# Kernel optimization log

Measured on AMD Instinct MI355X. Metric: run time of the kernel, lower is better.

Reference implementation:

```python
import jax, jax.numpy as jnp
import numpy as np
from jax import lax

WINDOW_SIZE = 11
SIGMA = 1.5
C1 = 0.01 ** 2
C2 = 0.03 ** 2


def _gaussian_window(channel, window_size, sigma=SIGMA):
    x = jnp.arange(window_size, dtype=jnp.float32)
    g = jnp.exp(-((x - window_size // 2) ** 2) / (2.0 * sigma * sigma))
    g = g / g.sum()
    w2d = jnp.outer(g, g)  # [ws, ws]
    # depthwise kernel in OIHW with feature_group_count=channel: [C, 1, ws, ws]
    return jnp.broadcast_to(w2d[None, None], (channel, 1, window_size, window_size))


def _dwconv(x, window, pad, channel):
    return lax.conv_general_dilated(
        x, window, window_strides=(1, 1), padding=[(pad, pad), (pad, pad)],
        dimension_numbers=("NCHW", "OIHW", "NCHW"), feature_group_count=channel)


def setup_inputs() -> dict:
    key = jax.random.key(0)
    k1, k2 = jax.random.split(key)
    shape = (16, 3, 512, 512)
    img1 = jax.random.uniform(k1, shape, dtype=jnp.float32)
    img2 = jax.random.uniform(k2, shape, dtype=jnp.float32)
    return {"img1": img1, "img2": img2}


def reference(img1, img2):
    _, channel, height, width = img1.shape
    ws = min(WINDOW_SIZE, height, width)
    window = _gaussian_window(channel, ws).astype(img1.dtype)
    pad = WINDOW_SIZE // 2  # matches torch code: padding=window_size // 2

    mu1 = _dwconv(img1, window, pad, channel)
    mu2 = _dwconv(img2, window, pad, channel)
    mu1_sq = mu1 * mu1
    mu2_sq = mu2 * mu2
    mu1_mu2 = mu1 * mu2

    sigma1_sq = _dwconv(img1 * img1, window, pad, channel) - mu1_sq
    sigma2_sq = _dwconv(img2 * img2, window, pad, channel) - mu2_sq
    sigma12 = _dwconv(img1 * img2, window, pad, channel) - mu1_mu2

    ssim_map = ((2.0 * mu1_mu2 + C1) * (2.0 * sigma12 + C2)) / (
        (mu1_sq + mu2_sq + C1) * (sigma1_sq + sigma2_sq + C2))
    return 1.0 - ssim_map.mean()
```

## Files before the change

kernel.cpp:

```cpp
#include <hip/hip_runtime.h>
#include <hip/hip_fp16.h>


#define IMGH 512
#define IMGW 512
#define TW 64
#define TH 32
#define HRR 42
#define C1F 1.0e-4f
#define C2F 9.0e-4f
#define GX 8
#define GY 16
#define GZ 48
#define NBLOCKS (GX * GY * GZ)
#define NPIX (16 * 3 * 512 * 512)

#define W0 0.0010283818f
#define W1 0.0075987503f
#define W2 0.0360007547f
#define W3 0.1093606960f
#define W4 0.2130055367f
#define W5 0.2660117184f

struct alignas(8) H4 { __half2 ab; __half2 qc; };

static __device__ __forceinline__ __half2 pkrtz(float a, float b) {
    auto r = __builtin_amdgcn_cvt_pkrtz(a, b);
    return *reinterpret_cast<__half2*>(&r);
}

__global__ __launch_bounds__(512, 4)
void ssim_tile(const float* __restrict__ img1, const float* __restrict__ img2,
               float* __restrict__ partials) {
    __shared__ H4 sPm[HRR][64];
    __shared__ float wsum[8];

    const float W[11] = {W0, W1, W2, W3, W4, W5, W4, W3, W2, W1, W0};
    __half2 wsH[11];
#pragma unroll
    for (int i = 0; i < 11; ++i) wsH[i] = __half2half2(__float2half(W[i]));

    const int tid = threadIdx.x;
    const int r0 = blockIdx.y * TH;
    const int c0 = blockIdx.x * TW;
    const size_t pbase = (size_t)blockIdx.z * (IMGH * IMGW);
    const float* a0 = img1 + pbase;
    const float* b0 = img2 + pbase;
    const bool fast = (blockIdx.x >= 1) & (blockIdx.x <= GX - 2) &
                      (blockIdx.y >= 1) & (blockIdx.y <= GY - 2);

    if (tid < HRR * 8) {
        const int row = tid >> 3;
        const int cg  = tid & 7;
        const int gr  = r0 - 5 + row;
        const bool rowok = (unsigned)gr < IMGH;
        const int grc = rowok ? gr : 0;
        const int gc0 = c0 + 8 * cg - 8;
        const float* ra = a0 + (size_t)grc * IMGW;
        const float* rb = b0 + (size_t)grc * IMGW;

        float4 va[6], vb[6];
        if (fast) {
#pragma unroll
            for (int g = 0; g < 6; ++g)
                va[g] = *reinterpret_cast<const float4*>(ra + (gc0 + 4 * g));
#pragma unroll
            for (int g = 0; g < 6; ++g)
                vb[g] = *reinterpret_cast<const float4*>(rb + (gc0 + 4 * g));
        } else {
#pragma unroll
            for (int g = 0; g < 6; ++g) {
                int gc = gc0 + 4 * g;
                va[g] = make_float4(0.f, 0.f, 0.f, 0.f); vb[g] = va[g];
                if (rowok && (unsigned)gc < IMGW) {
                    va[g] = *reinterpret_cast<const float4*>(ra + gc);
                    vb[g] = *reinterpret_cast<const float4*>(rb + gc);
                }
            }
        }

        __half2 AB[18], QC[18];
        auto emit = [&](int t, float a, float b) {
            AB[t] = pkrtz(a, b);
            QC[t] = pkrtz(__builtin_fmaf(a, a, b * b), a * b);
        };
        emit(0, va[0].w, vb[0].w);
#pragma unroll
        for (int g = 1; g < 6; ++g) {
            int t = 4 * g - 3;
            emit(t,     va[g].x, vb[g].x);
            emit(t + 1, va[g].y, vb[g].y);
            emit(t + 2, va[g].z, vb[g].z);
            if (g < 5) emit(t + 3, va[g].w, vb[g].w);
        }

        __half2 accAB[8], accQC[8];
        const __half2 z2 = __half2half2(__float2half(0.f));
#pragma unroll
        for (int m = 0; m < 8; ++m) { accAB[m] = z2; accQC[m] = z2; }
#pragma unroll
        for (int t = 0; t < 18; ++t) {
#pragma unroll
            for (int m = 0; m < 8; ++m) {
                int k = t - m;
                if (k >= 0 && k <= 10) {
                    accAB[m] = __hfma2(wsH[k], AB[t], accAB[m]);
                    accQC[m] = __hfma2(wsH[k], QC[t], accQC[m]);
                }
            }
        }
#pragma unroll
        for (int m = 0; m < 8; ++m) {
            H4 h; h.ab = accAB[m]; h.qc = accQC[m];
            sPm[row][8 * cg + m] = h;
        }
    }
    __syncthreads();

    const int col = tid & 63;
    const int rbase = (tid >> 6) * 4;
    const H4* pm = &sPm[rbase][col];

    __half2 mAB[4], mQC[4];
    {
        const __half2 z2 = __half2half2(__float2half(0.f));
#pragma unroll
        for (int r = 0; r < 4; ++r) { mAB[r] = z2; mQC[r] = z2; }
    }
#pragma unroll
    for (int j = 0; j < 14; ++j) {
        H4 h = pm[j * 64];
#pragma unroll
        for (int r = 0; r < 4; ++r) {
            int i = j - r;
            if (i >= 0 && i <= 10) {
                mAB[r] = __hfma2(wsH[i], h.ab, mAB[r]);
                mQC[r] = __hfma2(wsH[i], h.qc, mQC[r]);
            }
        }
    }

    float lsum = 0.f;
#pragma unroll
    for (int r = 0; r < 4; ++r) {
        float2 m12 = __half22float2(mAB[r]);
        float2 qc  = __half22float2(mQC[r]);
        float mu1 = m12.x, mu2 = m12.y;
        float mu11 = mu1 * mu1, mu22 = mu2 * mu2, mu12 = mu1 * mu2;
        float s12 = qc.y - mu12;
        float num = (2.f * mu12 + C1F) * (2.f * s12 + C2F);
        float den = (mu11 + mu22 + C1F) * ((qc.x - mu11 - mu22) + C2F);
        lsum += num * __builtin_amdgcn_rcpf(den);
    }

#pragma unroll
    for (int off = 32; off > 0; off >>= 1) lsum += __shfl_down(lsum, off, 64);
    if ((tid & 63) == 0) wsum[tid >> 6] = lsum;
    __syncthreads();
    if (tid == 0) {
        float t = 0.f;
#pragma unroll
        for (int w = 0; w < 8; ++w) t += wsum[w];
        partials[((size_t)blockIdx.z * GY + blockIdx.y) * GX + blockIdx.x] = t;
    }
}

__global__ __launch_bounds__(1024)
void ssim_reduce(const float* __restrict__ partials, float* __restrict__ out, int n) {
    __shared__ float lds[1024];
    float s = 0.f;
    for (int i = threadIdx.x; i < n; i += 1024) s += partials[i];
    lds[threadIdx.x] = s;
    __syncthreads();
    for (int off = 512; off > 0; off >>= 1) {
        if ((int)threadIdx.x < off) lds[threadIdx.x] += lds[threadIdx.x + off];
        __syncthreads();
    }
    if (threadIdx.x == 0) out[0] = 1.f - lds[0] / (float)NPIX;
}

extern "C" void kernel_launch(void* const* d_in, const int* in_sizes, int n_in,
                              void* d_out, int out_size, void* d_ws, size_t ws_size,
                              hipStream_t stream) {
    const float* img1 = (const float*)d_in[0];
    const float* img2 = (const float*)d_in[1];
    float* out = (float*)d_out;
    float* partials = (float*)d_ws;

    dim3 grid(GX, GY, GZ);
    ssim_tile<<<grid, 512, 0, stream>>>(img1, img2, partials);
    ssim_reduce<<<1, 1024, 0, stream>>>(partials, out, NBLOCKS);
}
```

Baseline: 45.23 us.

## Stage packed half2 input tile in LDS with coalesced loads before horizontal pass

Input loading is split into a cooperative phase where all 512 threads load float4s of both images, pack them to half2 and store them into a new LDS tile. The horizontal pass then reads its 24 inputs from LDS, which removes the redundant overlapping global loads per thread group. The squared and cross products are now computed in fp16 from the packed values, which reduces precision compared with the earlier fp32 products. LDS stores of the partial results are widened to float4. The cost is extra LDS usage and one more barrier.

```diff
diff --git a/kernel.cpp b/kernel.cpp
--- a/kernel.cpp
+++ b/kernel.cpp
@@ -7,6 +7,7 @@
 #define TW 64
 #define TH 32
 #define HRR 42
+#define SAB_STRIDE 84
 #define C1F 1.0e-4f
 #define C2F 9.0e-4f
 #define GX 8
@@ -32,6 +33,7 @@
 __global__ __launch_bounds__(512, 4)
 void ssim_tile(const float* __restrict__ img1, const float* __restrict__ img2,
                float* __restrict__ partials) {
+    __shared__ __half2 sAB[HRR][SAB_STRIDE];
     __shared__ H4 sPm[HRR][64];
     __shared__ float wsum[8];
 
@@ -49,50 +51,43 @@
     const bool fast = (blockIdx.x >= 1) & (blockIdx.x <= GX - 2) &
                       (blockIdx.y >= 1) & (blockIdx.y <= GY - 2);
 
+    for (int t = tid; t < HRR * 20; t += 512) {
+        int row = (unsigned)t / 20u;
+        int cq  = t - row * 20;
+        int gr  = r0 - 5 + row;
+        int gc  = c0 - 8 + 4 * cq;
+        __half2 h0, h1, h2, h3;
+        if (fast || ((unsigned)gr < IMGH && (unsigned)gc < IMGW)) {
+            const float4 va = *reinterpret_cast<const float4*>(
+                a0 + (size_t)gr * IMGW + gc);
+            const float4 vb = *reinterpret_cast<const float4*>(
+                b0 + (size_t)gr * IMGW + gc);
+            h0 = pkrtz(va.x, vb.x);
+            h1 = pkrtz(va.y, vb.y);
+            h2 = pkrtz(va.z, vb.z);
+            h3 = pkrtz(va.w, vb.w);
+        } else {
+            h0 = h1 = h2 = h3 = __half2half2(__float2half(0.f));
+        }
+        float4 st;
+        reinterpret_cast<__half2*>(&st)[0] = h0;
+        reinterpret_cast<__half2*>(&st)[1] = h1;
+        reinterpret_cast<__half2*>(&st)[2] = h2;
+        reinterpret_cast<__half2*>(&st)[3] = h3;
+        *reinterpret_cast<float4*>(&sAB[row][4 * cq]) = st;
+    }
+    __syncthreads();
+
     if (tid < HRR * 8) {
         const int row = tid >> 3;
         const int cg  = tid & 7;
-        const int gr  = r0 - 5 + row;
-        const bool rowok = (unsigned)gr < IMGH;
-        const int grc = rowok ? gr : 0;
-        const int gc0 = c0 + 8 * cg - 8;
-        const float* ra = a0 + (size_t)grc * IMGW;
-        const float* rb = b0 + (size_t)grc * IMGW;
+        const __half2* pr = &sAB[row][8 * cg];
 
-        float4 va[6], vb[6];
-        if (fast) {
+        __half2 A[24];
 #pragma unroll
-            for (int g = 0; g < 6; ++g)
-                va[g] = *reinterpret_cast<const float4*>(ra + (gc0 + 4 * g));
-#pragma unroll
-            for (int g = 0; g < 6; ++g)
-                vb[g] = *reinterpret_cast<const float4*>(rb + (gc0 + 4 * g));
-        } else {
-#pragma unroll
-            for (int g = 0; g < 6; ++g) {
-                int gc = gc0 + 4 * g;
-                va[g] = make_float4(0.f, 0.f, 0.f, 0.f); vb[g] = va[g];
-                if (rowok && (unsigned)gc < IMGW) {
-                    va[g] = *reinterpret_cast<const float4*>(ra + gc);
-                    vb[g] = *reinterpret_cast<const float4*>(rb + gc);
-                }
-            }
-        }
-
-        __half2 AB[18], QC[18];
-        auto emit = [&](int t, float a, float b) {
-            AB[t] = pkrtz(a, b);
-            QC[t] = pkrtz(__builtin_fmaf(a, a, b * b), a * b);
-        };
-        emit(0, va[0].w, vb[0].w);
-#pragma unroll
-        for (int g = 1; g < 6; ++g) {
-            int t = 4 * g - 3;
-            emit(t,     va[g].x, vb[g].x);
-            emit(t + 1, va[g].y, vb[g].y);
-            emit(t + 2, va[g].z, vb[g].z);
-            if (g < 5) emit(t + 3, va[g].w, vb[g].w);
-        }
+        for (int q = 0; q < 6; ++q)
+            *reinterpret_cast<float4*>(&A[4 * q]) =
+                *reinterpret_cast<const float4*>(&pr[4 * q]);
 
         __half2 accAB[8], accQC[8];
         const __half2 z2 = __half2half2(__float2half(0.f));
@@ -100,19 +95,28 @@
         for (int m = 0; m < 8; ++m) { accAB[m] = z2; accQC[m] = z2; }
 #pragma unroll
         for (int t = 0; t < 18; ++t) {
+            __half2 ab = A[t + 3];
+            __half2 q2 = __hmul2(ab, ab);
+            __half2 qc = __halves2half2(
+                __hadd(__low2half(q2), __high2half(q2)),
+                __hmul(__low2half(ab), __high2half(ab)));
 #pragma unroll
             for (int m = 0; m < 8; ++m) {
                 int k = t - m;
                 if (k >= 0 && k <= 10) {
-                    accAB[m] = __hfma2(wsH[k], AB[t], accAB[m]);
-                    accQC[m] = __hfma2(wsH[k], QC[t], accQC[m]);
+                    accAB[m] = __hfma2(wsH[k], ab, accAB[m]);
+                    accQC[m] = __hfma2(wsH[k], qc, accQC[m]);
                 }
             }
         }
 #pragma unroll
-        for (int m = 0; m < 8; ++m) {
-            H4 h; h.ab = accAB[m]; h.qc = accQC[m];
-            sPm[row][8 * cg + m] = h;
+        for (int m = 0; m < 8; m += 2) {
+            float4 st;
+            reinterpret_cast<__half2*>(&st)[0] = accAB[m];
+            reinterpret_cast<__half2*>(&st)[1] = accQC[m];
+            reinterpret_cast<__half2*>(&st)[2] = accAB[m + 1];
+            reinterpret_cast<__half2*>(&st)[3] = accQC[m + 1];
+            *reinterpret_cast<float4*>(&sPm[row][8 * cg + m]) = st;
         }
     }
     __syncthreads();
```

Result: slower. 53.62 us (+18.5%).

## Stage input tiles into LDS via direct global-to-LDS loads with swizzle

Applied to the files above, without the earlier changes.

Replaces the per-thread register float4 global loads of the halo tile with cooperative global_load_lds (16-byte) transfers into a swizzled shared staging buffer, then reads rows back from LDS. Border tiles zero-fill the stage first. The intent is to issue wider, better-coalesced memory traffic that bypasses VGPRs and to spread loads across all 512 threads instead of the 336 that compute. It also packs the horizontal-pass stores into 16-byte LDS writes. The cost is an extra ~27KB of LDS per block, which may reduce occupancy, plus an extra barrier and an extra LDS round-trip.

```diff
diff --git a/kernel.cpp b/kernel.cpp
--- a/kernel.cpp
+++ b/kernel.cpp
@@ -15,6 +15,10 @@
 #define NBLOCKS (GX * GY * GZ)
 #define NPIX (16 * 3 * 512 * 512)
 
+#define PLANE_W 3360
+#define STAGE_W 6912
+#define STAGE_BYTES 26880
+
 #define W0 0.0010283818f
 #define W1 0.0075987503f
 #define W2 0.0360007547f
@@ -29,9 +33,16 @@
     return *reinterpret_cast<__half2*>(&r);
 }
 
+static __device__ __forceinline__ void gload16(const void* g, void* l) {
+    __builtin_amdgcn_global_load_lds(
+        (const __attribute__((address_space(1))) void*)g,
+        (__attribute__((address_space(3))) void*)l, 16, 0, 0);
+}
+
 __global__ __launch_bounds__(512, 4)
 void ssim_tile(const float* __restrict__ img1, const float* __restrict__ img2,
                float* __restrict__ partials) {
+    __shared__ float stage[STAGE_W];
     __shared__ H4 sPm[HRR][64];
     __shared__ float wsum[8];
 
@@ -49,34 +60,46 @@
     const bool fast = (blockIdx.x >= 1) & (blockIdx.x <= GX - 2) &
                       (blockIdx.y >= 1) & (blockIdx.y <= GY - 2);
 
+    if (!fast) {
+        const float4 z4 = make_float4(0.f, 0.f, 0.f, 0.f);
+        for (int t = tid; t < STAGE_W / 4; t += 512)
+            reinterpret_cast<float4*>(stage)[t] = z4;
+        __syncthreads();
+    }
+    {
+        const int wv = tid >> 6, ln = tid & 63;
+        for (int i = wv; i < 27; i += 8) {
+            int o = (i << 10) + (ln << 4);
+            if (o < STAGE_BYTES) {
+                int plane = (o >= PLANE_W * 4) ? 1 : 0;
+                int po = o - plane * (PLANE_W * 4);
+                int row = (unsigned)po / 320u;
+                int ro  = po - row * 320;
+                ro ^= ((row >> 1) & 1) << 4;
+                int gr = r0 - 5 + row;
+                int gc = c0 - 8 + (ro >> 2);
+                if (fast || ((unsigned)gr < IMGH && (unsigned)gc < IMGW)) {
+                    const float* g = (plane ? b0 : a0) + (size_t)gr * IMGW + gc;
+                    gload16(g, reinterpret_cast<char*>(stage) + (i << 10));
+                }
+            }
+        }
+    }
+    __syncthreads();
+
     if (tid < HRR * 8) {
         const int row = tid >> 3;
         const int cg  = tid & 7;
-        const int gr  = r0 - 5 + row;
-        const bool rowok = (unsigned)gr < IMGH;
-        const int grc = rowok ? gr : 0;
-        const int gc0 = c0 + 8 * cg - 8;
-        const float* ra = a0 + (size_t)grc * IMGW;
-        const float* rb = b0 + (size_t)grc * IMGW;
+        const int s4  = ((row >> 1) & 1) << 2;
+        const float* pa = stage + row * 80 + cg * 8;
+        const float* pb = pa + PLANE_W;
 
         float4 va[6], vb[6];
-        if (fast) {
-#pragma unroll
-            for (int g = 0; g < 6; ++g)
-                va[g] = *reinterpret_cast<const float4*>(ra + (gc0 + 4 * g));
-#pragma unroll
-            for (int g = 0; g < 6; ++g)
-                vb[g] = *reinterpret_cast<const float4*>(rb + (gc0 + 4 * g));
-        } else {
-#pragma unroll
-            for (int g = 0; g < 6; ++g) {
-                int gc = gc0 + 4 * g;
-                va[g] = make_float4(0.f, 0.f, 0.f, 0.f); vb[g] = va[g];
-                if (rowok && (unsigned)gc < IMGW) {
-                    va[g] = *reinterpret_cast<const float4*>(ra + gc);
-                    vb[g] = *reinterpret_cast<const float4*>(rb + gc);
-                }
-            }
+#pragma unroll
+        for (int q = 0; q < 6; ++q) {
+            int off = ((q << 2) ^ s4);
+            va[q] = *reinterpret_cast<const float4*>(pa + off);
+            vb[q] = *reinterpret_cast<const float4*>(pb + off);
         }
 
         __half2 AB[18], QC[18];
@@ -110,9 +133,13 @@
             }
         }
 #pragma unroll
-        for (int m = 0; m < 8; ++m) {
-            H4 h; h.ab = accAB[m]; h.qc = accQC[m];
-            sPm[row][8 * cg + m] = h;
+        for (int m = 0; m < 8; m += 2) {
+            float4 st;
+            reinterpret_cast<__half2*>(&st)[0] = accAB[m];
+            reinterpret_cast<__half2*>(&st)[1] = accQC[m];
+            reinterpret_cast<__half2*>(&st)[2] = accAB[m + 1];
+            reinterpret_cast<__half2*>(&st)[3] = accQC[m + 1];
+            *reinterpret_cast<float4*>(&sPm[row][8 * cg + m]) = st;
         }
     }
     __syncthreads();
```

New measurement: 55.97 us. +23.7%, slower.

## Compute separable Gaussian convolutions with MFMA banded-matrix products

Applied to the files above, without the earlier changes.

Replaces the packed-half FMA horizontal and vertical 11-tap passes with MFMA 16x16x32 f16 matrix multiplies, using a banded Toeplitz weight matrix built from a zero-padded shared weight array. Inputs are staged into shared memory as four f16 planes (a, b, a²+b², ab), then transposed intermediate planes feed the vertical pass. The aim is to move the convolution arithmetic from vector ALUs onto the matrix cores. In exchange it uses more LDS, adds an extra barrier and layout transposes with possible bank conflicts, and relies on intricate fragment indexing.

```diff
diff --git a/kernel.cpp b/kernel.cpp
--- a/kernel.cpp
+++ b/kernel.cpp
@@ -6,14 +6,20 @@
 #define IMGW 512
 #define TW 64
 #define TH 32
-#define HRR 42
-#define C1F 1.0e-4f
-#define C2F 9.0e-4f
 #define GX 8
 #define GY 16
 #define GZ 48
 #define NBLOCKS (GX * GY * GZ)
 #define NPIX (16 * 3 * 512 * 512)
+#define C1F 1.0e-4f
+#define C2F 9.0e-4f
+
+#define INROWS 42
+#define INSTRIDE 88
+#define INPLANE (INROWS * INSTRIDE)
+#define VSTRIDE 44
+#define VPLANE (64 * VSTRIDE)
+#define WBASE 34
 
 #define W0 0.0010283818f
 #define W1 0.0075987503f
@@ -22,7 +28,8 @@
 #define W4 0.2130055367f
 #define W5 0.2660117184f
 
-struct alignas(8) H4 { __half2 ab; __half2 qc; };
+typedef _Float16 half8v __attribute__((ext_vector_type(8)));
+typedef float f32x4 __attribute__((ext_vector_type(4)));
 
 static __device__ __forceinline__ __half2 pkrtz(float a, float b) {
     auto r = __builtin_amdgcn_cvt_pkrtz(a, b);
@@ -32,15 +39,14 @@
 __global__ __launch_bounds__(512, 4)
 void ssim_tile(const float* __restrict__ img1, const float* __restrict__ img2,
                float* __restrict__ partials) {
-    __shared__ H4 sPm[HRR][64];
+    __shared__ _Float16 sWext[96];
+    __shared__ _Float16 sIn[4 * INPLANE];
+    __shared__ _Float16 sV[4 * VPLANE];
     __shared__ float wsum[8];
 
-    const float W[11] = {W0, W1, W2, W3, W4, W5, W4, W3, W2, W1, W0};
-    __half2 wsH[11];
-#pragma unroll
-    for (int i = 0; i < 11; ++i) wsH[i] = __half2half2(__float2half(W[i]));
-
-    const int tid = threadIdx.x;
+    const int tid  = threadIdx.x;
+    const int lane = tid & 63;
+    const int wv   = tid >> 6;
     const int r0 = blockIdx.y * TH;
     const int c0 = blockIdx.x * TW;
     const size_t pbase = (size_t)blockIdx.z * (IMGH * IMGW);
@@ -49,113 +55,112 @@
     const bool fast = (blockIdx.x >= 1) & (blockIdx.x <= GX - 2) &
                       (blockIdx.y >= 1) & (blockIdx.y <= GY - 2);
 
-    if (tid < HRR * 8) {
-        const int row = tid >> 3;
-        const int cg  = tid & 7;
-        const int gr  = r0 - 5 + row;
-        const bool rowok = (unsigned)gr < IMGH;
-        const int grc = rowok ? gr : 0;
-        const int gc0 = c0 + 8 * cg - 8;
-        const float* ra = a0 + (size_t)grc * IMGW;
-        const float* rb = b0 + (size_t)grc * IMGW;
+    if (tid < 96) {
+        const float W[11] = {W0, W1, W2, W3, W4, W5, W4, W3, W2, W1, W0};
+        float w = 0.f;
+#pragma unroll
+        for (int j = 0; j < 11; ++j) w = (tid == WBASE + j) ? W[j] : w;
+        sWext[tid] = (_Float16)w;
+    }
 
-        float4 va[6], vb[6];
-        if (fast) {
+    auto prep = [&](int qid) {
+        const int row = qid / 20;
+        const int cq  = qid - row * 20;
+        const int gr = r0 - 5 + row;
+        const int gc = c0 - 8 + 4 * cq;
+        float4 va = make_float4(0.f, 0.f, 0.f, 0.f), vb = va;
+        if (fast || ((unsigned)gr < IMGH && (unsigned)gc < IMGW)) {
+            va = *reinterpret_cast<const float4*>(a0 + (size_t)gr * IMGW + gc);
+            vb = *reinterpret_cast<const float4*>(b0 + (size_t)gr * IMGW + gc);
+        }
+        const int off = row * INSTRIDE + 4 * cq;
+        auto st = [&](int plane, __half2 lo, __half2 hi) {
+            uint2 u;
+            u.x = *reinterpret_cast<const unsigned*>(&lo);
+            u.y = *reinterpret_cast<const unsigned*>(&hi);
+            *reinterpret_cast<uint2*>(&sIn[plane * INPLANE + off]) = u;
+        };
+        st(0, pkrtz(va.x, va.y), pkrtz(va.z, va.w));
+        st(1, pkrtz(vb.x, vb.y), pkrtz(vb.z, vb.w));
+        float q0 = __builtin_fmaf(va.x, va.x, vb.x * vb.x);
+        float q1 = __builtin_fmaf(va.y, va.y, vb.y * vb.y);
+        float q2 = __builtin_fmaf(va.z, va.z, vb.z * vb.z);
+        float q3 = __builtin_fmaf(va.w, va.w, vb.w * vb.w);
+        st(2, pkrtz(q0, q1), pkrtz(q2, q3));
+        st(3, pkrtz(va.x * vb.x, va.y * vb.y),
+              pkrtz(va.z * vb.z, va.w * vb.w));
+    };
+    prep(tid);
+    if (tid < 840 - 512) prep(tid + 512);
+    __syncthreads();
+
+    const int rt2 = wv >> 2;
+    half8v Ah, Av;
+    {
+        const int bh = ((lane >> 4) << 3) - (lane & 15) - 3 + WBASE;
+        const int bv = ((lane >> 4) << 3) - (lane & 15) - (rt2 ? 6 : 0) + WBASE;
 #pragma unroll
-            for (int g = 0; g < 6; ++g)
-                va[g] = *reinterpret_cast<const float4*>(ra + (gc0 + 4 * g));
+        for (int e = 0; e < 8; ++e) Ah[e] = sWext[bh + e];
 #pragma unroll
-            for (int g = 0; g < 6; ++g)
-                vb[g] = *reinterpret_cast<const float4*>(rb + (gc0 + 4 * g));
-        } else {
+        for (int e = 0; e < 8; ++e) Av[e] = sWext[bv + e];
+    }
+
 #pragma unroll
-            for (int g = 0; g < 6; ++g) {
-                int gc = gc0 + 4 * g;
-                va[g] = make_float4(0.f, 0.f, 0.f, 0.f); vb[g] = va[g];
-                if (rowok && (unsigned)gc < IMGW) {
-                    va[g] = *reinterpret_cast<const float4*>(ra + gc);
-                    vb[g] = *reinterpret_cast<const float4*>(rb + gc);
-                }
+    for (int i = 0; i < 6; ++i) {
+        const int id = wv + (i << 3);
+        const int rt = id >> 4;
+        const int ct = (id >> 2) & 3;
+        const int q  = id & 3;
+        const int rb = (rt == 0) ? 0 : (rt == 1 ? 16 : 26);
+        const int row = rb + (lane & 15);
+        const int colstart = 16 * ct + ((lane >> 4) << 3);
+        const half8v b = *reinterpret_cast<const half8v*>(
+            &sIn[q * INPLANE + row * INSTRIDE + colstart]);
+        f32x4 d = {0.f, 0.f, 0.f, 0.f};
+        d = __builtin_amdgcn_mfma_f32_16x16x32_f16(Ah, b, d, 0, 0, 0);
+        if (rt < 2 || (lane & 15) >= 6) {
+#pragma unroll
+            for (int j = 0; j < 4; ++j) {
+                const int oc = 16 * ct + ((lane >> 4) << 2) + j;
+                sV[q * VPLANE + oc * VSTRIDE + row] = (_Float16)d[j];
             }
-        }
-
-        __half2 AB[18], QC[18];
-        auto emit = [&](int t, float a, float b) {
-            AB[t] = pkrtz(a, b);
-            QC[t] = pkrtz(__builtin_fmaf(a, a, b * b), a * b);
-        };
-        emit(0, va[0].w, vb[0].w);
-#pragma unroll
-        for (int g = 1; g < 6; ++g) {
-            int t = 4 * g - 3;
-            emit(t,     va[g].x, vb[g].x);
-            emit(t + 1, va[g].y, vb[g].y);
-            emit(t + 2, va[g].z, vb[g].z);
-            if (g < 5) emit(t + 3, va[g].w, vb[g].w);
-        }
-
-        __half2 accAB[8], accQC[8];
-        const __half2 z2 = __half2half2(__float2half(0.f));
-#pragma unroll
-        for (int m = 0; m < 8; ++m) { accAB[m] = z2; accQC[m] = z2; }
-#pragma unroll
-        for (int t = 0; t < 18; ++t) {
-#pragma unroll
-            for (int m = 0; m < 8; ++m) {
-                int k = t - m;
-                if (k >= 0 && k <= 10) {
-                    accAB[m] = __hfma2(wsH[k], AB[t], accAB[m]);
-                    accQC[m] = __hfma2(wsH[k], QC[t], accQC[m]);
-                }
-            }
-        }
-#pragma unroll
-        for (int m = 0; m < 8; ++m) {
-            H4 h; h.ab = accAB[m]; h.qc = accQC[m];
-            sPm[row][8 * cg + m] = h;
         }
     }
     __syncthreads();
 
-    const int col = tid & 63;
-    const int rbase = (tid >> 6) * 4;
-    const H4* pm = &sPm[rbase][col];
-
-    __half2 mAB[4], mQC[4];
-    {
-        const __half2 z2 = __half2half2(__float2half(0.f));
-#pragma unroll
-        for (int r = 0; r < 4; ++r) { mAB[r] = z2; mQC[r] = z2; }
-    }
-#pragma unroll
-    for (int j = 0; j < 14; ++j) {
-        H4 h = pm[j * 64];
-#pragma unroll
-        for (int r = 0; r < 4; ++r) {
-            int i = j - r;
-            if (i >= 0 && i <= 10) {
-                mAB[r] = __hfma2(wsH[i], h.ab, mAB[r]);
-                mQC[r] = __hfma2(wsH[i], h.qc, mQC[r]);
-            }
-        }
-    }
+    const int ct2 = wv & 3;
+    const int w0 = rt2 ? 10 : 0;
+    const int vcol = 16 * ct2 + (lane & 15);
+    const int rowst = w0 + ((lane >> 4) << 3);
+    auto vread = [&](int q) -> half8v {
+        const _Float16* p = &sV[q * VPLANE + vcol * VSTRIDE + rowst];
+        union { unsigned u[4]; half8v h; } c;
+        c.u[0] = *reinterpret_cast<const unsigned*>(p);
+        c.u[1] = *reinterpret_cast<const unsigned*>(p + 2);
+        c.u[2] = *reinterpret_cast<const unsigned*>(p + 4);
+        c.u[3] = *reinterpret_cast<const unsigned*>(p + 6);
+        return c.h;
+    };
+    f32x4 d0 = {0.f, 0.f, 0.f, 0.f}, d1 = d0, d2 = d0, d3 = d0;
+    d0 = __builtin_amdgcn_mfma_f32_16x16x32_f16(Av, vread(0), d0, 0, 0, 0);
+    d1 = __builtin_amdgcn_mfma_f32_16x16x32_f16(Av, vread(1), d1, 0, 0, 0);
+    d2 = __builtin_amdgcn_mfma_f32_16x16x32_f16(Av, vread(2), d2, 0, 0, 0);
+    d3 = __builtin_amdgcn_mfma_f32_16x16x32_f16(Av, vread(3), d3, 0, 0, 0);
 
     float lsum = 0.f;
 #pragma unroll
     for (int r = 0; r < 4; ++r) {
-        float2 m12 = __half22float2(mAB[r]);
-        float2 qc  = __half22float2(mQC[r]);
-        float mu1 = m12.x, mu2 = m12.y;
-        float mu11 = mu1 * mu1, mu22 = mu2 * mu2, mu12 = mu1 * mu2;
-        float s12 = qc.y - mu12;
-        float num = (2.f * mu12 + C1F) * (2.f * s12 + C2F);
-        float den = (mu11 + mu22 + C1F) * ((qc.x - mu11 - mu22) + C2F);
+        const float mu1 = d0[r], mu2 = d1[r], S = d2[r], eab = d3[r];
+        const float mu11 = mu1 * mu1, mu22 = mu2 * mu2, mu12 = mu1 * mu2;
+        const float s12 = eab - mu12;
+        const float num = (2.f * mu12 + C1F) * (2.f * s12 + C2F);
+        const float den = (mu11 + mu22 + C1F) * ((S - mu11 - mu22) + C2F);
         lsum += num * __builtin_amdgcn_rcpf(den);
     }
 
 #pragma unroll
     for (int off = 32; off > 0; off >>= 1) lsum += __shfl_down(lsum, off, 64);
-    if ((tid & 63) == 0) wsum[tid >> 6] = lsum;
+    if (lane == 0) wsum[wv] = lsum;
     __syncthreads();
     if (tid == 0) {
         float t = 0.f;
```

Result: slower. 52.04 us (+15.1%).
